# Kernel optimization log

Hardware: AMD Instinct MI355X
Metric: run time of the kernel (lower is better)

## Reference

```python
import jax, jax.numpy as jnp
import numpy as np

NUM_HEADS = 16
NUM_KV_HEADS = 8
HEAD_DIM = 128
HIDDEN = 2048
Q_SIZE = NUM_HEADS * HEAD_DIM          # 2048
KV_SIZE = NUM_KV_HEADS * HEAD_DIM      # 1024
SCALING = 256.0 ** -0.5                # query_pre_attn_scalar ** -0.5
EPS = 1e-6
BATCH = 8
ENC_LEN = 512                          # encoder_len_per_req
Q_LEN = 2048                           # sum of extend_seq_lens (8 * 256)
KV_LEN = BATCH * ENC_LEN               # 4096


def _rms_norm(x, w):
    # Gemma3RMSNorm: fp32 compute, scale by (1 + weight)
    xf = x.astype(jnp.float32)
    xf = xf * jax.lax.rsqrt(jnp.mean(xf * xf, axis=-1, keepdims=True) + EPS)
    return (xf * (1.0 + w.astype(jnp.float32))).astype(x.dtype)


def setup_inputs() -> dict:
    key = jax.random.key(0)
    k1, k2, k3 = jax.random.split(key, 3)
    return {
        "hidden_states": jax.random.normal(k1, (Q_LEN, HIDDEN), jnp.float32),
        "encoder_hidden_states": jax.random.normal(k2, (KV_LEN, HIDDEN), jnp.float32),
        "w_qkv": jax.random.normal(k3, (Q_SIZE + 2 * KV_SIZE, HIDDEN), jnp.float32) * 0.02,
        "q_norm_w": jnp.zeros((HEAD_DIM,), jnp.float32),
        "k_norm_w": jnp.zeros((HEAD_DIM,), jnp.float32),
        "seq_lens": jnp.full((BATCH,), Q_LEN // BATCH, jnp.int32),  # extend_seq_lens per request
    }


def reference(hidden_states, encoder_hidden_states, w_qkv, q_norm_w, k_norm_w, seq_lens):
    # decoder side: only q is used
    qkv_dec = hidden_states @ w_qkv.T                     # [q_len, 4096]
    q = qkv_dec[:, :Q_SIZE].reshape(Q_LEN, NUM_HEADS, HEAD_DIM)
    q = _rms_norm(q, q_norm_w) * SCALING

    # encoder side: only k, v are used
    qkv_enc = encoder_hidden_states @ w_qkv.T             # [kv_len, 4096]
    k = qkv_enc[:, Q_SIZE:Q_SIZE + KV_SIZE].reshape(KV_LEN, NUM_KV_HEADS, HEAD_DIM)
    v = qkv_enc[:, Q_SIZE + KV_SIZE:].reshape(KV_LEN, NUM_KV_HEADS, HEAD_DIM)
    k = _rms_norm(k, k_norm_w)

    # GQA: repeat each kv head n_rep times (consecutively, matching expand+reshape)
    n_rep = NUM_HEADS // NUM_KV_HEADS
    k = jnp.repeat(k, n_rep, axis=1)                      # [kv_len, H, D]
    v = jnp.repeat(v, n_rep, axis=1)

    # scores per head: [H, q_len, kv_len]
    scores = jnp.einsum('qhd,khd->hqk', q, k)

    # ragged block-diagonal mask: query token i belongs to request r iff
    # cumsum(seq_lens)[r-1] <= i < cumsum(seq_lens)[r]; kv token j -> j // ENC_LEN
    q_req = jnp.searchsorted(jnp.cumsum(seq_lens), jnp.arange(Q_LEN), side='right')
    kv_req = jnp.arange(KV_LEN) // ENC_LEN
    mask = q_req[:, None] == kv_req[None, :]              # [q_len, kv_len] bool
    scores = jnp.where(mask[None, :, :], scores, -jnp.inf)

    attn = jax.nn.softmax(scores.astype(jnp.float32), axis=-1).astype(v.dtype)
    out = jnp.einsum('hqk,khd->qhd', attn, v)             # [q_len, H, D]
    return out.reshape(Q_LEN, NUM_HEADS * HEAD_DIM)
```

## Files before the change

### kernel.cpp

```cpp
#include <hip/hip_runtime.h>

typedef __attribute__((ext_vector_type(8))) short short8;
typedef __attribute__((ext_vector_type(4))) float f32x4;

#define DEVI __device__ __forceinline__

static constexpr int HIDDEN   = 2048;
static constexpr int NHEADS   = 16;
static constexpr int NKV      = 8;
static constexpr int HDIM     = 128;
static constexpr int QLEN     = 2048;
static constexpr int KVLEN    = 4096;
static constexpr int ENCLEN   = 512;
static constexpr int NREQ     = 8;
static constexpr float SCALING = 0.0625f;
static constexpr float EPS     = 1e-6f;

DEVI unsigned short f2bf(float f) {
  unsigned int b = __float_as_uint(f);
  b += 0x7FFFu + ((b >> 16) & 1u);
  return (unsigned short)(b >> 16);
}

DEVI void g2l16(const void* g, void* l) {
  __builtin_amdgcn_global_load_lds(
      (const __attribute__((address_space(1))) void*)g,
      (__attribute__((address_space(3))) void*)l, 16, 0, 0);
}

__global__ __launch_bounds__(256) void cvt_all(const float* __restrict__ h,
                                               const float* __restrict__ e,
                                               const float* __restrict__ w,
                                               unsigned short* __restrict__ hb,
                                               unsigned short* __restrict__ eb,
                                               unsigned short* __restrict__ wb) {
  constexpr long S1 = (long)2048 * 2048, S2 = (long)4096 * 2048;
  long i = ((long)blockIdx.x * 256 + threadIdx.x) * 8;
  const float* src;
  unsigned short* dst;
  if (i < S1)           { src = h + i;            dst = hb + i; }
  else if (i < S1 + S2) { src = e + (i - S1);     dst = eb + (i - S1); }
  else                  { src = w + (i - S1 - S2); dst = wb + (i - S1 - S2); }
  float4 a = *(const float4*)src;
  float4 b = *(const float4*)(src + 4);
  short8 o;
  o[0] = (short)f2bf(a.x); o[1] = (short)f2bf(a.y);
  o[2] = (short)f2bf(a.z); o[3] = (short)f2bf(a.w);
  o[4] = (short)f2bf(b.x); o[5] = (short)f2bf(b.y);
  o[6] = (short)f2bf(b.z); o[7] = (short)f2bf(b.w);
  *(short8*)dst = o;
}


#define LGKM0 { asm volatile("s_waitcnt lgkmcnt(0)" ::: "memory"); __builtin_amdgcn_sched_barrier(0); }
#define VM4   { asm volatile("s_waitcnt vmcnt(4)" ::: "memory"); __builtin_amdgcn_sched_barrier(0); }
#define VM0   { asm volatile("s_waitcnt vmcnt(0)" ::: "memory"); __builtin_amdgcn_sched_barrier(0); }
#define SBAR  __builtin_amdgcn_s_barrier()

DEVI short8 rdfrag(const char* unit, int row, int lg) {
  int L = row >> 1;
  int g = ((row & 1) << 2) + lg;
  return *(const short8*)(unit + L * 128 + ((g ^ (L & 7)) << 4));
}

__global__ __launch_bounds__(512, 2) void gemm_qkv8(
    const unsigned short* __restrict__ Adec, const unsigned short* __restrict__ Aenc,
    const unsigned short* __restrict__ Bw,
    const float* __restrict__ q_nw, const float* __restrict__ k_nw,
    unsigned short* __restrict__ q_bf, unsigned short* __restrict__ k_bf,
    unsigned short* __restrict__ v_t) {
  extern __shared__ char lds[];
  const int K = 2048, NT = 32;

  int flat = blockIdx.y * 8 + blockIdx.x;
  int swz = (flat & 7) * 24 + (flat >> 3);
  int bx = swz & 7, by = swz >> 3;

  const unsigned short* A;
  int bm0;
  if (by < 8) { A = Adec; bm0 = by * 256; }
  else        { A = Aenc; bm0 = (by - 8) * 256; }
  const unsigned short* Bp = Bw + (by < 8 ? 0 : (size_t)2048 * 2048);
  const int bn0 = bx * 256;

  const int tid = threadIdx.x, lane = tid & 63, wave = tid >> 6;
  const int lr = lane & 15, lg = lane >> 4;
  const int wr = wave >> 2, wc = wave & 3;
  const int bq = (wc & 1) * 64;

#define AU(b, kk, h) (lds + ((((b)*2 + (kk)) * 2 + (h)) << 13))
#define BU(b, kk, h) (lds + 65536 + ((((b)*2 + (kk)) * 2 + (h)) << 13))

  const int sB = tid * 16;
  const int sL = sB >> 7, sgp = (sB >> 4) & 7;
  const int sg = sgp ^ (sL & 7);
  const int st_row = sL * 2 + (sg >> 2);
  const int st_col = (sg & 3) * 8;
  const size_t a0off = (size_t)(bm0 + st_row) * K + st_col;
  const size_t a1off = a0off + (size_t)128 * K;
  const size_t b0off = (size_t)(bn0 + st_row) * K + st_col;
  const size_t b1off = b0off + (size_t)128 * K;

#define STG(srcp, ubase) g2l16((srcp), (ubase) + sB)

  f32x4 acc[8][4] = {};
  short8 a[4], b[4];

#define DS_A(cur, kkc, mq)                                          \
  {                                                                 \
    const char* u = AU(cur, kkc, wr);                               \
    _Pragma("unroll") for (int m = 0; m < 4; ++m)                   \
        a[m] = rdfrag(u, (mq)*64 + m * 16 + lr, lg);                \
  }
#define DS_B(cur, kkc)                                              \
  {                                                                 \
    const char* u = BU(cur, kkc, wc >> 1);                          \
    _Pragma("unroll") for (int n = 0; n < 4; ++n)                   \
        b[n] = rdfrag(u, bq + n * 16 + lr, lg);                     \
  }
#define MFMA16(mq)                                                  \
  {                                                                 \
    __builtin_amdgcn_s_setprio(1);                                  \
    _Pragma("unroll") for (int m = 0; m < 4; ++m)                   \
        _Pragma("unroll") for (int n = 0; n < 4; ++n)               \
            acc[(mq)*4 + m][n] = __builtin_amdgcn_mfma_f32_16x16x32_bf16( \
                a[m], b[n], acc[(mq)*4 + m][n], 0, 0, 0);           \
    __builtin_amdgcn_s_setprio(0);                                  \
  }

  STG(A + a0off, AU(0, 0, 0));  STG(A + a1off, AU(0, 0, 1));
  STG(Bp + b0off, BU(0, 0, 0)); STG(Bp + b1off, BU(0, 0, 1));
  STG(A + a0off + 32, AU(0, 1, 0));  STG(A + a1off + 32, AU(0, 1, 1));
  STG(Bp + b0off + 32, BU(0, 1, 0)); STG(Bp + b1off + 32, BU(0, 1, 1));
  VM4; SBAR;

  int cur = 0;
  for (int kt = 0; kt < NT - 1; ++kt) {
    const int nb = cur ^ 1;
    const size_t kn = (size_t)(kt + 1) * 64;
    DS_A(cur, 0, 0); DS_B(cur, 0);
    STG(A + a0off + kn, AU(nb, 0, 0)); STG(A + a1off + kn, AU(nb, 0, 1));
    LGKM0; MFMA16(0); SBAR;
    DS_A(cur, 0, 1);
    STG(Bp + b0off + kn, BU(nb, 0, 0)); STG(Bp + b1off + kn, BU(nb, 0, 1));
    LGKM0; MFMA16(1); VM4; SBAR;
    DS_A(cur, 1, 0); DS_B(cur, 1);
    STG(A + a0off + kn + 32, AU(nb, 1, 0)); STG(A + a1off + kn + 32, AU(nb, 1, 1));
    LGKM0; MFMA16(0); SBAR;
    DS_A(cur, 1, 1);
    STG(Bp + b0off + kn + 32, BU(nb, 1, 0)); STG(Bp + b1off + kn + 32, BU(nb, 1, 1));
    LGKM0; MFMA16(1); VM4; SBAR;
    cur = nb;
  }
  DS_A(cur, 0, 0); DS_B(cur, 0); LGKM0; MFMA16(0); SBAR;
  DS_A(cur, 0, 1);               LGKM0; MFMA16(1); VM0; SBAR;
  DS_A(cur, 1, 0); DS_B(cur, 1); LGKM0; MFMA16(0); SBAR;
  DS_A(cur, 1, 1);               LGKM0; MFMA16(1);

  const int btype = (by < 8) ? 0 : (bx < 4 ? 1 : 2);
  const int tokbase0 = (by < 8 ? by : by - 8) * 256;

  if (btype < 2) {
    float* Lf = (float*)lds;
    const float* wnorm = (btype == 0) ? q_nw : k_nw;
    const float fscale = (btype == 0) ? SCALING : 1.0f;
    unsigned short* dst = (btype == 0) ? q_bf : k_bf;
    const size_t LEN = (btype == 0) ? (size_t)QLEN : (size_t)KVLEN;
    const int dloc = lr * 8;
    float wv[8];
#pragma unroll
    for (int j = 0; j < 8; ++j) wv[j] = 1.0f + wnorm[dloc + j];

#pragma unroll
    for (int q = 0; q < 4; ++q) {
      SBAR;
      if (wr == (q >> 1)) {
        const int amb = (q & 1) * 4;
#pragma unroll
        for (int am2 = 0; am2 < 4; ++am2)
#pragma unroll
          for (int n = 0; n < 4; ++n)
#pragma unroll
            for (int r = 0; r < 4; ++r)
              Lf[(am2 * 16 + lg * 4 + r) * 260 + wc * 64 + n * 16 + lr] =
                  acc[amb + am2][n][r];
      }
      SBAR;
#pragma unroll
      for (int it = 0; it < 4; ++it) {
        int pair = it * 32 + wave * 4 + (lane >> 4);
        int row = pair >> 1, hh = pair & 1;
        const float* src = &Lf[row * 260 + hh * 128 + dloc];
        f32x4 x0 = *(const f32x4*)src;
        f32x4 x1 = *(const f32x4*)(src + 4);
        float ssq = x0[0]*x0[0] + x0[1]*x0[1] + x0[2]*x0[2] + x0[3]*x0[3] +
                    x1[0]*x1[0] + x1[1]*x1[1] + x1[2]*x1[2] + x1[3]*x1[3];
#pragma unroll
        for (int m = 8; m >= 1; m >>= 1) ssq += __shfl_xor(ssq, m);
        float sc = rsqrtf(ssq * (1.0f / 128.0f) + EPS) * fscale;
        short8 o;
        o[0] = (short)f2bf(x0[0] * sc * wv[0]); o[1] = (short)f2bf(x0[1] * sc * wv[1]);
        o[2] = (short)f2bf(x0[2] * sc * wv[2]); o[3] = (short)f2bf(x0[3] * sc * wv[3]);
        o[4] = (short)f2bf(x1[0] * sc * wv[4]); o[5] = (short)f2bf(x1[1] * sc * wv[5]);
        o[6] = (short)f2bf(x1[2] * sc * wv[6]); o[7] = (short)f2bf(x1[3] * sc * wv[7]);
        int tok = tokbase0 + q * 64 + row;
        int hd = 2 * bx + hh;
        *(short8*)&dst[((size_t)hd * LEN + tok) * 128 + dloc] = o;
      }
    }
  } else {
    float* Lv = (float*)lds;
#pragma unroll
    for (int q = 0; q < 4; ++q) {
      SBAR;
      if (wr == (q >> 1)) {
        const int amb = (q & 1) * 4;
#pragma unroll
        for (int am2 = 0; am2 < 4; ++am2)
#pragma unroll
          for (int n = 0; n < 4; ++n)
            *(f32x4*)&Lv[(wc * 64 + n * 16 + lr) * 68 + am2 * 16 + lg * 4] =
                acc[amb + am2][n];
      }
      SBAR;
      int d = tid >> 1, th = tid & 1;
      const float* src = &Lv[d * 68 + th * 32];
      int kh = (bx - 4) * 2 + (d >> 7);
      int tok = tokbase0 + q * 64 + th * 32;
      unsigned short* vp = &v_t[((size_t)kh * 128 + (d & 127)) * KVLEN + tok];
#pragma unroll
      for (int j = 0; j < 4; ++j) {
        f32x4 v0 = *(const f32x4*)(src + j * 8);
        f32x4 v1 = *(const f32x4*)(src + j * 8 + 4);
        short8 o;
        o[0] = (short)f2bf(v0[0]); o[1] = (short)f2bf(v0[1]);
        o[2] = (short)f2bf(v0[2]); o[3] = (short)f2bf(v0[3]);
        o[4] = (short)f2bf(v1[0]); o[5] = (short)f2bf(v1[1]);
        o[6] = (short)f2bf(v1[2]); o[7] = (short)f2bf(v1[3]);
        *(short8*)(vp + j * 8) = o;
      }
    }
  }
#undef AU
#undef BU
#undef STG
#undef DS_A
#undef DS_B
#undef MFMA16
}

__global__ __launch_bounds__(256, 4) void attn_kernel(
    const unsigned short* __restrict__ qb,
    const unsigned short* __restrict__ kb,
    const unsigned short* __restrict__ vt,
    const int* __restrict__ seq_lens,
    unsigned short* __restrict__ Opart,
    float* __restrict__ mlpart) {
  __shared__ __align__(16) unsigned short Ks[64 * 128];
  __shared__ __align__(16) unsigned short Vs[128 * 64];
  __shared__ __align__(16) unsigned short Ps[64 * 64];

  const int h = blockIdx.y, split = blockIdx.z;
  const int t0 = blockIdx.x * 64;
  int req = 0, qs = 0;
#pragma unroll 1
  while (req < NREQ - 1 && qs + seq_lens[req] <= t0) { qs += seq_lens[req]; ++req; }
  const int slen = seq_lens[req];
  const int rows = min(64, qs + slen - t0);
  if (rows <= 0) return;
  const int qbase = t0;

  const int tid = threadIdx.x, lane = tid & 63, wave = tid >> 6;
  const int lr = lane & 15, lg = lane >> 4;
  const int m0w = wave * 16;
  const int kh = h >> 1;
  const int kv0 = req * ENCLEN + split * (ENCLEN / 2);

  short8 a_q[4];
  {
    int qr = qbase + min(m0w + lr, rows - 1);
    const unsigned short* qp = qb + ((size_t)h * QLEN + qr) * 128 + lg * 8;
#pragma unroll
    for (int ks = 0; ks < 4; ++ks) a_q[ks] = *(const short8*)(qp + ks * 32);
  }

  f32x4 acc[8] = {};
  float mrow[4], lsum[4];
#pragma unroll
  for (int r = 0; r < 4; ++r) { mrow[r] = -1e30f; lsum[r] = 0.f; }

  for (int c = 0; c < 4; ++c) {
#pragma unroll
    for (int i = 0; i < 4; ++i) {
      int idx = i * 256 + tid;
      int row = idx >> 4, slot = idx & 15;
      g2l16(kb + ((size_t)kh * KVLEN + kv0 + c * 64 + row) * 128 + ((slot ^ (row & 15)) << 3),
            &Ks[idx * 8]);
    }
#pragma unroll
    for (int i = 0; i < 4; ++i) {
      int idx = i * 256 + tid;
      int row = idx >> 3, slot = idx & 7;
      g2l16(vt + ((size_t)kh * 128 + row) * KVLEN + kv0 + c * 64 + ((slot ^ (row & 7)) << 3),
            &Vs[idx * 8]);
    }
    __syncthreads();

    f32x4 s[4] = {};
#pragma unroll
    for (int ks = 0; ks < 4; ++ks) {
      short8 bk[4];
#pragma unroll
      for (int n = 0; n < 4; ++n) {
        int row = n * 16 + lr;
        bk[n] = *(const short8*)&Ks[row * 128 + (((ks * 4 + lg) ^ (row & 15)) << 3)];
      }
#pragma unroll
      for (int n = 0; n < 4; ++n)
        s[n] = __builtin_amdgcn_mfma_f32_16x16x32_bf16(a_q[ks], bk[n], s[n], 0, 0, 0);
    }

#pragma unroll
    for (int r = 0; r < 4; ++r) {
      float mx = fmaxf(fmaxf(s[0][r], s[1][r]), fmaxf(s[2][r], s[3][r]));
#pragma unroll
      for (int msk = 8; msk >= 1; msk >>= 1) mx = fmaxf(mx, __shfl_xor(mx, msk));
      float mnew = fmaxf(mrow[r], mx);
      float al = __expf(mrow[r] - mnew);
      mrow[r] = mnew;
      float rs = 0.f;
#pragma unroll
      for (int n = 0; n < 4; ++n) {
        float p = __expf(s[n][r] - mnew);
        s[n][r] = p;
        rs += p;
      }
#pragma unroll
      for (int msk = 8; msk >= 1; msk >>= 1) rs += __shfl_xor(rs, msk);
      lsum[r] = lsum[r] * al + rs;
#pragma unroll
      for (int n2 = 0; n2 < 8; ++n2) acc[n2][r] *= al;
    }

#pragma unroll
    for (int n = 0; n < 4; ++n)
#pragma unroll
      for (int r = 0; r < 4; ++r) {
        int row = m0w + lg * 4 + r;
        int col = n * 16 + lr;
        Ps[row * 64 + (col ^ ((row & 7) << 3))] = f2bf(s[n][r]);
      }
    asm volatile("s_waitcnt lgkmcnt(0)" ::: "memory");
    __builtin_amdgcn_sched_barrier(0);

#pragma unroll
    for (int ks = 0; ks < 2; ++ks) {
      int prow = m0w + lr;
      short8 pa = *(const short8*)&Ps[prow * 64 + (((ks * 4 + lg) ^ (prow & 7)) << 3)];
#pragma unroll
      for (int n2 = 0; n2 < 8; ++n2) {
        int row = n2 * 16 + lr;
        short8 bv = *(const short8*)&Vs[row * 64 + (((ks * 4 + lg) ^ (row & 7)) << 3)];
        acc[n2] = __builtin_amdgcn_mfma_f32_16x16x32_bf16(pa, bv, acc[n2], 0, 0, 0);
      }
    }
    __syncthreads();
  }

  if (lr == 0) {
#pragma unroll
    for (int r = 0; r < 4; ++r) {
      int row = m0w + lg * 4 + r;
      if (row < rows) {
        float2 v = make_float2(mrow[r], lsum[r]);
        *(float2*)&mlpart[(((size_t)split * 16 + h) * QLEN + qbase + row) * 2] = v;
      }
    }
  }

  constexpr int OFS = 132;
  float* Of = (float*)Ks;
#pragma unroll
  for (int n2 = 0; n2 < 8; ++n2)
#pragma unroll
    for (int r = 0; r < 4; ++r)
      Of[(m0w + lg * 4 + r) * OFS + n2 * 16 + lr] = acc[n2][r];
  __syncthreads();
#pragma unroll
  for (int p = 0; p < 4; ++p) {
    int idx = p * 256 + tid;
    int row = idx >> 4, ch = idx & 15;
    if (row < rows) {
      const float* src = &Of[row * OFS + ch * 8];
      f32x4 v0 = *(const f32x4*)src;
      f32x4 v1 = *(const f32x4*)(src + 4);
      short8 o;
      o[0] = (short)f2bf(v0[0]); o[1] = (short)f2bf(v0[1]);
      o[2] = (short)f2bf(v0[2]); o[3] = (short)f2bf(v0[3]);
      o[4] = (short)f2bf(v1[0]); o[5] = (short)f2bf(v1[1]);
      o[6] = (short)f2bf(v1[2]); o[7] = (short)f2bf(v1[3]);
      *(short8*)&Opart[(((size_t)split * 16 + h) * QLEN + qbase + row) * 128 + ch * 8] = o;
    }
  }
}

__global__ __launch_bounds__(256) void combine_kernel(const unsigned short* __restrict__ Opart,
                                                      const float* __restrict__ mlpart,
                                                      float* __restrict__ out) {
  int w = blockIdx.x * 4 + (threadIdx.x >> 6);
  int lane = threadIdx.x & 63;
  int h = w >> 11, q = w & 2047;
  float2 ml0 = *(const float2*)&mlpart[((size_t)h * QLEN + q) * 2];
  float2 ml1 = *(const float2*)&mlpart[(((size_t)16 + h) * QLEN + q) * 2];
  float M = fmaxf(ml0.x, ml1.x);
  float c0 = __expf(ml0.x - M), c1 = __expf(ml1.x - M);
  float inv = 1.0f / (c0 * ml0.y + c1 * ml1.y);
  unsigned int u0 = *(const unsigned int*)&Opart[((size_t)h * QLEN + q) * 128 + lane * 2];
  unsigned int u1 = *(const unsigned int*)&Opart[(((size_t)16 + h) * QLEN + q) * 128 + lane * 2];
  float a0 = __uint_as_float(u0 << 16),  b0 = __uint_as_float(u0 & 0xFFFF0000u);
  float a1 = __uint_as_float(u1 << 16),  b1 = __uint_as_float(u1 & 0xFFFF0000u);
  float2 r;
  r.x = (c0 * a0 + c1 * a1) * inv;
  r.y = (c0 * b0 + c1 * b1) * inv;
  *(float2*)&out[(size_t)q * 2048 + h * 128 + lane * 2] = r;
}

extern "C" void kernel_launch(void* const* d_in, const int* in_sizes, int n_in,
                              void* d_out, int out_size, void* d_ws, size_t ws_size,
                              hipStream_t stream) {
  const float* hidden = (const float*)d_in[0];
  const float* enc    = (const float*)d_in[1];
  const float* w_qkv  = (const float*)d_in[2];
  const float* q_nw   = (const float*)d_in[3];
  const float* k_nw   = (const float*)d_in[4];
  const int*   slens  = (const int*)d_in[5];
  float* out = (float*)d_out;

  char* ws = (char*)d_ws;
  unsigned short* h_bf = (unsigned short*)(ws + 0);
  unsigned short* e_bf = (unsigned short*)(ws + 8388608);
  unsigned short* w_bf = (unsigned short*)(ws + 25165824);
  unsigned short* q_bf = (unsigned short*)(ws + 41943040);
  unsigned short* k_bf = (unsigned short*)(ws + 50331648);
  unsigned short* v_t  = (unsigned short*)(ws + 58720256);
  unsigned short* Opart = (unsigned short*)(ws + 67108864);
  float* mlpart = (float*)(ws + 83886080);

  static bool attr_set = false;
  if (!attr_set) {
    hipFuncSetAttribute((const void*)gemm_qkv8,
                        hipFuncAttributeMaxDynamicSharedMemorySize, 131072);
    attr_set = true;
  }

  cvt_all<<<10240, 256, 0, stream>>>(hidden, enc, w_qkv, h_bf, e_bf, w_bf);

  gemm_qkv8<<<dim3(8, 24), 512, 131072, stream>>>(h_bf, e_bf, w_bf, q_nw, k_nw,
                                                  q_bf, k_bf, v_t);

  attn_kernel<<<dim3(32, 16, 2), 256, 0, stream>>>(q_bf, k_bf, v_t, slens, Opart, mlpart);
  combine_kernel<<<8192, 256, 0, stream>>>(Opart, mlpart, out);
}
```

Baseline: 121.9 us.

## Deepen GEMM prefetch to 4 LDS slots and drop split-KV attention combine

The QKV GEMM replaces its double-buffered k-tile scheme with a 4-slot ring of half-tiles, so global-to-LDS loads run further ahead (waitcnt relaxed to 8 outstanding). The attention kernel no longer splits each request's 512 KV tokens into two halves. Each block now processes all 8 chunks, normalizes by the row sum in-kernel and writes fp32 output directly. This removes the combine kernel launch and the bf16 partial-output round trip, at the cost of half as many attention blocks (512), which reduces parallelism on the GPU.

```diff
diff --git a/kernel.cpp b/kernel.cpp
--- a/kernel.cpp
+++ b/kernel.cpp
@@ -53,6 +53,7 @@
 
 
 #define LGKM0 { asm volatile("s_waitcnt lgkmcnt(0)" ::: "memory"); __builtin_amdgcn_sched_barrier(0); }
+#define VM8   { asm volatile("s_waitcnt vmcnt(8)" ::: "memory"); __builtin_amdgcn_sched_barrier(0); }
 #define VM4   { asm volatile("s_waitcnt vmcnt(4)" ::: "memory"); __builtin_amdgcn_sched_barrier(0); }
 #define VM0   { asm volatile("s_waitcnt vmcnt(0)" ::: "memory"); __builtin_amdgcn_sched_barrier(0); }
 #define SBAR  __builtin_amdgcn_s_barrier()
@@ -88,8 +89,9 @@
   const int wr = wave >> 2, wc = wave & 3;
   const int bq = (wc & 1) * 64;
 
-#define AU(b, kk, h) (lds + ((((b)*2 + (kk)) * 2 + (h)) << 13))
-#define BU(b, kk, h) (lds + 65536 + ((((b)*2 + (kk)) * 2 + (h)) << 13))
+#define SLOT(kt, kk) ((((kt) << 1) | (kk)) & 3)
+#define AUs(s, h) (lds + ((((s) << 1) | (h)) << 13))
+#define BUs(s, h) (lds + 65536 + ((((s) << 1) | (h)) << 13))
 
   const int sB = tid * 16;
   const int sL = sB >> 7, sgp = (sB >> 4) & 7;
@@ -102,19 +104,26 @@
   const size_t b1off = b0off + (size_t)128 * K;
 
 #define STG(srcp, ubase) g2l16((srcp), (ubase) + sB)
+#define STG4(kt, kk)                                                \
+  {                                                                 \
+    const size_t kc = (size_t)(kt) * 64 + (kk) * 32;                \
+    const int s_ = SLOT(kt, kk);                                    \
+    STG(A + a0off + kc, AUs(s_, 0));  STG(A + a1off + kc, AUs(s_, 1)); \
+    STG(Bp + b0off + kc, BUs(s_, 0)); STG(Bp + b1off + kc, BUs(s_, 1)); \
+  }
 
   f32x4 acc[8][4] = {};
   short8 a[4], b[4];
 
-#define DS_A(cur, kkc, mq)                                          \
+#define DS_A(s, mq)                                                 \
   {                                                                 \
-    const char* u = AU(cur, kkc, wr);                               \
+    const char* u = AUs(s, wr);                                     \
     _Pragma("unroll") for (int m = 0; m < 4; ++m)                   \
         a[m] = rdfrag(u, (mq)*64 + m * 16 + lr, lg);                \
   }
-#define DS_B(cur, kkc)                                              \
+#define DS_B(s)                                                     \
   {                                                                 \
-    const char* u = BU(cur, kkc, wc >> 1);                          \
+    const char* u = BUs(s, wc >> 1);                                \
     _Pragma("unroll") for (int n = 0; n < 4; ++n)                   \
         b[n] = rdfrag(u, bq + n * 16 + lr, lg);                     \
   }
@@ -128,34 +137,30 @@
     __builtin_amdgcn_s_setprio(0);                                  \
   }
 
-  STG(A + a0off, AU(0, 0, 0));  STG(A + a1off, AU(0, 0, 1));
-  STG(Bp + b0off, BU(0, 0, 0)); STG(Bp + b1off, BU(0, 0, 1));
-  STG(A + a0off + 32, AU(0, 1, 0));  STG(A + a1off + 32, AU(0, 1, 1));
-  STG(Bp + b0off + 32, BU(0, 1, 0)); STG(Bp + b1off + 32, BU(0, 1, 1));
-  VM4; SBAR;
-
-  int cur = 0;
-  for (int kt = 0; kt < NT - 1; ++kt) {
-    const int nb = cur ^ 1;
-    const size_t kn = (size_t)(kt + 1) * 64;
-    DS_A(cur, 0, 0); DS_B(cur, 0);
-    STG(A + a0off + kn, AU(nb, 0, 0)); STG(A + a1off + kn, AU(nb, 0, 1));
-    LGKM0; MFMA16(0); SBAR;
-    DS_A(cur, 0, 1);
-    STG(Bp + b0off + kn, BU(nb, 0, 0)); STG(Bp + b1off + kn, BU(nb, 0, 1));
-    LGKM0; MFMA16(1); VM4; SBAR;
-    DS_A(cur, 1, 0); DS_B(cur, 1);
-    STG(A + a0off + kn + 32, AU(nb, 1, 0)); STG(A + a1off + kn + 32, AU(nb, 1, 1));
-    LGKM0; MFMA16(0); SBAR;
-    DS_A(cur, 1, 1);
-    STG(Bp + b0off + kn + 32, BU(nb, 1, 0)); STG(Bp + b1off + kn + 32, BU(nb, 1, 1));
-    LGKM0; MFMA16(1); VM4; SBAR;
-    cur = nb;
-  }
-  DS_A(cur, 0, 0); DS_B(cur, 0); LGKM0; MFMA16(0); SBAR;
-  DS_A(cur, 0, 1);               LGKM0; MFMA16(1); VM0; SBAR;
-  DS_A(cur, 1, 0); DS_B(cur, 1); LGKM0; MFMA16(0); SBAR;
-  DS_A(cur, 1, 1);               LGKM0; MFMA16(1);
+  STG4(0, 0); STG4(0, 1); STG4(1, 0);
+  VM8; SBAR;
+
+  for (int kt = 0; kt < NT - 2; ++kt) {
+    const int s0 = SLOT(kt, 0), s1 = SLOT(kt, 1);
+    DS_A(s0, 0); DS_B(s0); STG4(kt + 1, 1); LGKM0; MFMA16(0); SBAR;
+    DS_A(s0, 1);                            LGKM0; MFMA16(1); VM8; SBAR;
+    DS_A(s1, 0); DS_B(s1); STG4(kt + 2, 0); LGKM0; MFMA16(0); SBAR;
+    DS_A(s1, 1);                            LGKM0; MFMA16(1); VM8; SBAR;
+  }
+  {
+    const int s0 = SLOT(NT - 2, 0), s1 = SLOT(NT - 2, 1);
+    DS_A(s0, 0); DS_B(s0); STG4(NT - 1, 1); LGKM0; MFMA16(0); SBAR;
+    DS_A(s0, 1);                            LGKM0; MFMA16(1); VM8; SBAR;
+    DS_A(s1, 0); DS_B(s1);                  LGKM0; MFMA16(0); SBAR;
+    DS_A(s1, 1);                            LGKM0; MFMA16(1); VM4; SBAR;
+  }
+  {
+    const int s0 = SLOT(NT - 1, 0), s1 = SLOT(NT - 1, 1);
+    DS_A(s0, 0); DS_B(s0); LGKM0; MFMA16(0); SBAR;
+    DS_A(s0, 1);           LGKM0; MFMA16(1); VM0; SBAR;
+    DS_A(s1, 0); DS_B(s1); LGKM0; MFMA16(0); SBAR;
+    DS_A(s1, 1);           LGKM0; MFMA16(1);
+  }
 
   const int btype = (by < 8) ? 0 : (bx < 4 ? 1 : 2);
   const int tokbase0 = (by < 8 ? by : by - 8) * 256;
@@ -241,9 +246,11 @@
       }
     }
   }
-#undef AU
-#undef BU
+#undef SLOT
+#undef AUs
+#undef BUs
 #undef STG
+#undef STG4
 #undef DS_A
 #undef DS_B
 #undef MFMA16
@@ -254,13 +261,12 @@
     const unsigned short* __restrict__ kb,
     const unsigned short* __restrict__ vt,
     const int* __restrict__ seq_lens,
-    unsigned short* __restrict__ Opart,
-    float* __restrict__ mlpart) {
+    float* __restrict__ out) {
   __shared__ __align__(16) unsigned short Ks[64 * 128];
   __shared__ __align__(16) unsigned short Vs[128 * 64];
   __shared__ __align__(16) unsigned short Ps[64 * 64];
 
-  const int h = blockIdx.y, split = blockIdx.z;
+  const int h = blockIdx.y;
   const int t0 = blockIdx.x * 64;
   int req = 0, qs = 0;
 #pragma unroll 1
@@ -274,7 +280,7 @@
   const int lr = lane & 15, lg = lane >> 4;
   const int m0w = wave * 16;
   const int kh = h >> 1;
-  const int kv0 = req * ENCLEN + split * (ENCLEN / 2);
+  const int kv0 = req * ENCLEN;
 
   short8 a_q[4];
   {
@@ -289,7 +295,7 @@
 #pragma unroll
   for (int r = 0; r < 4; ++r) { mrow[r] = -1e30f; lsum[r] = 0.f; }
 
-  for (int c = 0; c < 4; ++c) {
+  for (int c = 0; c < 8; ++c) {
 #pragma unroll
     for (int i = 0; i < 4; ++i) {
       int idx = i * 256 + tid;
@@ -367,16 +373,13 @@
     __syncthreads();
   }
 
-  if (lr == 0) {
-#pragma unroll
-    for (int r = 0; r < 4; ++r) {
-      int row = m0w + lg * 4 + r;
-      if (row < rows) {
-        float2 v = make_float2(mrow[r], lsum[r]);
-        *(float2*)&mlpart[(((size_t)split * 16 + h) * QLEN + qbase + row) * 2] = v;
-      }
-    }
-  }
+  float inv[4];
+#pragma unroll
+  for (int r = 0; r < 4; ++r) inv[r] = 1.0f / lsum[r];
+#pragma unroll
+  for (int n2 = 0; n2 < 8; ++n2)
+#pragma unroll
+    for (int r = 0; r < 4; ++r) acc[n2][r] *= inv[r];
 
   constexpr int OFS = 132;
   float* Of = (float*)Ks;
@@ -387,42 +390,14 @@
       Of[(m0w + lg * 4 + r) * OFS + n2 * 16 + lr] = acc[n2][r];
   __syncthreads();
 #pragma unroll
-  for (int p = 0; p < 4; ++p) {
+  for (int p = 0; p < 8; ++p) {
     int idx = p * 256 + tid;
-    int row = idx >> 4, ch = idx & 15;
+    int row = idx >> 5, c4 = (idx & 31) * 4;
     if (row < rows) {
-      const float* src = &Of[row * OFS + ch * 8];
-      f32x4 v0 = *(const f32x4*)src;
-      f32x4 v1 = *(const f32x4*)(src + 4);
-      short8 o;
-      o[0] = (short)f2bf(v0[0]); o[1] = (short)f2bf(v0[1]);
-      o[2] = (short)f2bf(v0[2]); o[3] = (short)f2bf(v0[3]);
-      o[4] = (short)f2bf(v1[0]); o[5] = (short)f2bf(v1[1]);
-      o[6] = (short)f2bf(v1[2]); o[7] = (short)f2bf(v1[3]);
-      *(short8*)&Opart[(((size_t)split * 16 + h) * QLEN + qbase + row) * 128 + ch * 8] = o;
-    }
-  }
-}
-
-__global__ __launch_bounds__(256) void combine_kernel(const unsigned short* __restrict__ Opart,
-                                                      const float* __restrict__ mlpart,
-                                                      float* __restrict__ out) {
-  int w = blockIdx.x * 4 + (threadIdx.x >> 6);
-  int lane = threadIdx.x & 63;
-  int h = w >> 11, q = w & 2047;
-  float2 ml0 = *(const float2*)&mlpart[((size_t)h * QLEN + q) * 2];
-  float2 ml1 = *(const float2*)&mlpart[(((size_t)16 + h) * QLEN + q) * 2];
-  float M = fmaxf(ml0.x, ml1.x);
-  float c0 = __expf(ml0.x - M), c1 = __expf(ml1.x - M);
-  float inv = 1.0f / (c0 * ml0.y + c1 * ml1.y);
-  unsigned int u0 = *(const unsigned int*)&Opart[((size_t)h * QLEN + q) * 128 + lane * 2];
-  unsigned int u1 = *(const unsigned int*)&Opart[(((size_t)16 + h) * QLEN + q) * 128 + lane * 2];
-  float a0 = __uint_as_float(u0 << 16),  b0 = __uint_as_float(u0 & 0xFFFF0000u);
-  float a1 = __uint_as_float(u1 << 16),  b1 = __uint_as_float(u1 & 0xFFFF0000u);
-  float2 r;
-  r.x = (c0 * a0 + c1 * a1) * inv;
-  r.y = (c0 * b0 + c1 * b1) * inv;
-  *(float2*)&out[(size_t)q * 2048 + h * 128 + lane * 2] = r;
+      f32x4 v = *(const f32x4*)&Of[row * OFS + c4];
+      *(f32x4*)&out[(size_t)(qbase + row) * 2048 + h * 128 + c4] = v;
+    }
+  }
 }
 
 extern "C" void kernel_launch(void* const* d_in, const int* in_sizes, int n_in,
@@ -443,8 +418,6 @@
   unsigned short* q_bf = (unsigned short*)(ws + 41943040);
   unsigned short* k_bf = (unsigned short*)(ws + 50331648);
   unsigned short* v_t  = (unsigned short*)(ws + 58720256);
-  unsigned short* Opart = (unsigned short*)(ws + 67108864);
-  float* mlpart = (float*)(ws + 83886080);
 
   static bool attr_set = false;
   if (!attr_set) {
@@ -458,6 +431,5 @@
   gemm_qkv8<<<dim3(8, 24), 512, 131072, stream>>>(h_bf, e_bf, w_bf, q_nw, k_nw,
                                                   q_bf, k_bf, v_t);
 
-  attn_kernel<<<dim3(32, 16, 2), 256, 0, stream>>>(q_bf, k_bf, v_t, slens, Opart, mlpart);
-  combine_kernel<<<8192, 256, 0, stream>>>(Opart, mlpart, out);
-}
+  attn_kernel<<<dim3(32, 16), 256, 0, stream>>>(q_bf, k_bf, v_t, slens, out);
+}
```

Result: faster. 116.2 us (-4.7%).
